# Kernel optimization log

Measured on AMD Instinct MI355X. Metric: run time of the kernel, lower is better.

Reference implementation:

```python
import jax, jax.numpy as jnp
import numpy as np

KS = 3   # deform conv kernel size
PAD = 1  # deform conv padding


def conv2d(x, w, b=None, stride=1, pad=0):
    out = jax.lax.conv_general_dilated(
        x, w, (stride, stride), [(pad, pad), (pad, pad)],
        dimension_numbers=('NCHW', 'OIHW', 'NCHW'))
    if b is not None:
        out = out + b[None, :, None, None]
    return out


def batchnorm(x, g, b, eps=1e-5):
    # training-mode BN (batch statistics, biased variance) like torch default
    m = jnp.mean(x, axis=(0, 2, 3), keepdims=True)
    v = jnp.var(x, axis=(0, 2, 3), keepdims=True)
    return (x - m) * jax.lax.rsqrt(v + eps) * g[None, :, None, None] + b[None, :, None, None]


def deform_conv(x, offset, w):
    # x: (b,c,h,w); offset: (b,2N,h,w) with first N = x-offsets, last N = y-offsets
    b, c, h, wd = x.shape
    N = KS * KS
    xp = jnp.pad(x, ((0, 0), (0, 0), (PAD, PAD), (PAD, PAD)))
    Hp, Wp = h + 2 * PAD, wd + 2 * PAD
    # kernel-point offsets p_n in {-1,0,1}^2
    r = jnp.arange(-(KS - 1) // 2, (KS - 1) // 2 + 1)
    pnx, pny = jnp.meshgrid(r, r, indexing='ij')
    p_n = jnp.concatenate([pnx.reshape(-1), pny.reshape(-1)]).astype(x.dtype)  # (2N,)
    # base sampling grid p_0 (1..h, 1..w in padded coords)
    p0x, p0y = jnp.meshgrid(jnp.arange(1, h + 1), jnp.arange(1, wd + 1), indexing='ij')
    p0 = jnp.concatenate([jnp.broadcast_to(p0x[None], (N, h, wd)),
                          jnp.broadcast_to(p0y[None], (N, h, wd))], 0).astype(x.dtype)
    p = p0[None] + p_n[None, :, None, None] + offset          # (b,2N,h,w)
    p = jnp.transpose(p, (0, 2, 3, 1))                        # (b,h,w,2N)
    px, py = p[..., :N], p[..., N:]
    fx, fy = jnp.floor(px), jnp.floor(py)
    q_ltx = jnp.clip(fx, 0, Hp - 1)
    q_lty = jnp.clip(fy, 0, Wp - 1)
    q_rbx = jnp.clip(fx + 1, 0, Hp - 1)
    q_rby = jnp.clip(fy + 1, 0, Wp - 1)
    # out-of-bound positions snapped to floor, then clamped (matches torch ref)
    mx = (px < PAD) | (px > Hp - 1 - PAD)
    my = (py < PAD) | (py > Wp - 1 - PAD)
    px = jnp.clip(jnp.where(mx, fx, px), 0, Hp - 1)
    py = jnp.clip(jnp.where(my, fy, py), 0, Wp - 1)
    g_lt = (1 + (q_ltx - px)) * (1 + (q_lty - py))
    g_rb = (1 - (q_rbx - px)) * (1 - (q_rby - py))
    g_lb = (1 + (q_ltx - px)) * (1 - (q_rby - py))
    g_rt = (1 - (q_rbx - px)) * (1 + (q_lty - py))
    x_flat = xp.reshape(b, c, Hp * Wp)

    def gather(qx, qy):
        idx = (qx.astype(jnp.int32) * Wp + qy.astype(jnp.int32)).reshape(b, 1, -1)
        out = jnp.take_along_axis(x_flat, jnp.broadcast_to(idx, (b, c, idx.shape[-1])), axis=2)
        return out.reshape(b, c, h, wd, N)

    x_off = (g_lt[:, None] * gather(q_ltx, q_lty)
             + g_rb[:, None] * gather(q_rbx, q_rby)
             + g_lb[:, None] * gather(q_ltx, q_rby)
             + g_rt[:, None] * gather(q_rbx, q_lty))   # (b,c,h,w,N)
    # (b,c,h,w,ki,kj) -> (b,c,h*ks,w*ks), then conv with stride ks
    x_off = x_off.reshape(b, c, h, wd, KS, KS).transpose(0, 1, 2, 4, 3, 5).reshape(b, c, h * KS, wd * KS)
    return conv2d(x_off, w, None, stride=KS, pad=0)


def setup_inputs() -> dict:
    key = jax.random.key(0)
    ks = jax.random.split(key, 6)
    f32 = jnp.float32
    x = jax.random.normal(ks[0], (4, 3, 224, 224), f32)
    conv1_w = jax.random.normal(ks[1], (64, 3, 3, 3), f32) * (1.0 / np.sqrt(3 * 9))
    conv1_b = jnp.zeros((64,), f32)
    bn1_g = jnp.ones((64,), f32); bn1_b = jnp.zeros((64,), f32)
    conv2_w = jax.random.normal(ks[2], (128, 64, 3, 3), f32) * (1.0 / np.sqrt(64 * 9))
    conv2_b = jnp.zeros((128,), f32)
    bn2_g = jnp.ones((128,), f32); bn2_b = jnp.zeros((128,), f32)
    off_w = jax.random.normal(ks[3], (18, 128, 3, 3), f32) * 0.01
    off_b = jnp.zeros((18,), f32)
    conv4_w = jax.random.normal(ks[4], (128, 128, 3, 3), f32) * (1.0 / np.sqrt(128 * 9))
    return {'x': x, 'conv1_w': conv1_w, 'conv1_b': conv1_b, 'bn1_g': bn1_g, 'bn1_b': bn1_b,
            'conv2_w': conv2_w, 'conv2_b': conv2_b, 'bn2_g': bn2_g, 'bn2_b': bn2_b,
            'off_w': off_w, 'off_b': off_b, 'conv4_w': conv4_w}


def reference(x, conv1_w, conv1_b, bn1_g, bn1_b, conv2_w, conv2_b, bn2_g, bn2_b, off_w, off_b, conv4_w):
    h = jax.nn.relu(conv2d(x, conv1_w, conv1_b, pad=1))
    h = batchnorm(h, bn1_g, bn1_b)
    b_, c_, H, W = h.shape
    h = h.reshape(b_, c_, H // 2, 2, W // 2, 2).mean(axis=(3, 5))  # AvgPool2d(2,2)
    h = jax.nn.relu(conv2d(h, conv2_w, conv2_b, pad=1))
    h = batchnorm(h, bn2_g, bn2_b)
    offsets = conv2d(h, off_w, off_b, pad=1)
    return deform_conv(h, offsets, conv4_w)
```

## Files before the change

### kernel.cpp

```cpp
#include <hip/hip_runtime.h>

#define HW1 50176
#define HW2 12544

typedef short bf16x8 __attribute__((ext_vector_type(8)));
typedef float f32x4  __attribute__((ext_vector_type(4)));

static __device__ __forceinline__ unsigned short f2bf(float f) {
  union { float f; unsigned int u; } v; v.f = f;
  unsigned int u = v.u;
  return (unsigned short)((u + 0x7fffu + ((u >> 16) & 1u)) >> 16);
}
static __device__ __forceinline__ float bf2f(unsigned short h) {
  union { unsigned int u; float f; } v; v.u = ((unsigned int)h) << 16;
  return v.f;
}

__global__ __launch_bounds__(256) void prep_kernel(
    const float* __restrict__ conv4_w, const float* __restrict__ conv2_w,
    const float* __restrict__ off_w,
    unsigned short* __restrict__ wbf, unsigned short* __restrict__ wb2h,
    unsigned short* __restrict__ wb2l, unsigned short* __restrict__ wboh,
    unsigned short* __restrict__ wbol)
{
  int t = blockIdx.x * 256 + threadIdx.x;
  if (t < 147456) {
    int o = t / 1152, r = t % 1152;
    int kk = r / 128, c = r % 128;
    wbf[t] = f2bf(conv4_w[((size_t)o * 128 + c) * 9 + kk]);
  }
  int t2 = t - 147456;
  if (t2 >= 0 && t2 < 73728) {
    int o = t2 / 576, r = t2 % 576;
    int kk = r / 64, c = r % 64;
    float v = conv2_w[((size_t)o * 64 + c) * 9 + kk];
    unsigned short h = f2bf(v);
    wb2h[t2] = h; wb2l[t2] = f2bf(v - bf2f(h));
  }
  int t3 = t - (147456 + 73728);
  if (t3 >= 0 && t3 < 36864) {
    int o = t3 / 1152, r = t3 % 1152;
    int kk = r / 128, c = r % 128;
    float v = (o < 18) ? off_w[((size_t)o * 128 + c) * 9 + kk] : 0.f;
    unsigned short h = f2bf(v);
    wboh[t3] = h; wbol[t3] = f2bf(v - bf2f(h));
  }
}

__global__ __launch_bounds__(256) void conv1_tiled_kernel(
    const float* __restrict__ x, const float* __restrict__ w,
    const float* __restrict__ bias, float* __restrict__ out)
{
  __shared__ float in_s[3][18][18];
  int tid = threadIdx.x;
  int tx = tid & 15, ty = tid >> 4;
  int tx0 = (blockIdx.x % 14) * 16, ty0 = (blockIdx.x / 14) * 16;
  int b = blockIdx.y;

  for (int t = tid; t < 972; t += 256) {
    int c = t / 324, r2 = t % 324;
    int r = r2 / 18, col = r2 % 18;
    int yy = ty0 + r - 1, xx = tx0 + col - 1;
    float v = 0.f;
    if (yy >= 0 && yy < 224 && xx >= 0 && xx < 224)
      v = x[((size_t)(b * 3 + c) * 224 + yy) * 224 + xx];
    in_s[c][r][col] = v;
  }
  __syncthreads();

  float xv[27];
  #pragma unroll
  for (int c = 0; c < 3; ++c)
    #pragma unroll
    for (int ky = 0; ky < 3; ++ky)
      #pragma unroll
      for (int kx = 0; kx < 3; ++kx)
        xv[c * 9 + ky * 3 + kx] = in_s[c][ty + ky][tx + kx];

  int oy = ty0 + ty, ox = tx0 + tx;
  size_t obase = ((size_t)b * 64) * HW1 + (size_t)oy * 224 + ox;
  for (int o0 = 0; o0 < 64; o0 += 16) {
    float acc[16];
    #pragma unroll
    for (int oi = 0; oi < 16; ++oi) acc[oi] = bias[o0 + oi];
    #pragma unroll
    for (int oi = 0; oi < 16; ++oi) {
      const float* wp = w + (size_t)(o0 + oi) * 27;
      #pragma unroll
      for (int k = 0; k < 27; ++k)
        acc[oi] += xv[k] * wp[k];
    }
    #pragma unroll
    for (int oi = 0; oi < 16; ++oi)
      out[obase + (size_t)(o0 + oi) * HW1] = fmaxf(acc[oi], 0.f);
  }
}

__global__ __launch_bounds__(256) void bn_stats_part_kernel(
    const float* __restrict__ in, float* __restrict__ part, int C, int HW)
{
  int c = blockIdx.y;
  int NB = gridDim.x;
  float s = 0.f, s2 = 0.f;
  int stride = NB * 256;
  int start = blockIdx.x * 256 + threadIdx.x;
  for (int b = 0; b < 4; ++b) {
    const float* p = in + (size_t)(b * C + c) * HW;
    for (int i = start; i < HW; i += stride) {
      float v = p[i];
      s += v; s2 += v * v;
    }
  }
  #pragma unroll
  for (int off = 32; off > 0; off >>= 1) {
    s  += __shfl_down(s, off, 64);
    s2 += __shfl_down(s2, off, 64);
  }
  __shared__ float red[8];
  int wid = threadIdx.x >> 6, lane = threadIdx.x & 63;
  if (lane == 0) { red[wid * 2] = s; red[wid * 2 + 1] = s2; }
  __syncthreads();
  if (threadIdx.x == 0) {
    float ts = 0.f, ts2 = 0.f;
    for (int i = 0; i < 4; ++i) { ts += red[i * 2]; ts2 += red[i * 2 + 1]; }
    part[((size_t)c * NB + blockIdx.x) * 2]     = ts;
    part[((size_t)c * NB + blockIdx.x) * 2 + 1] = ts2;
  }
}

__global__ void bn_finalize_kernel(const float* __restrict__ part, int NB,
                                   const float* __restrict__ g,
                                   const float* __restrict__ bb,
                                   float inv_n, float* __restrict__ ss, int C)
{
  int c = threadIdx.x;
  if (c < C) {
    float s = 0.f, s2 = 0.f;
    for (int i = 0; i < NB; ++i) {
      s  += part[((size_t)c * NB + i) * 2];
      s2 += part[((size_t)c * NB + i) * 2 + 1];
    }
    float m = s * inv_n;
    float v = s2 * inv_n - m * m;
    float sc = rsqrtf(v + 1e-5f) * g[c];
    ss[2 * c] = sc;
    ss[2 * c + 1] = bb[c] - m * sc;
  }
}

__global__ __launch_bounds__(256) void bn1_pool_nhwc_kernel(
    const float* __restrict__ h1, const float* __restrict__ ss,
    float* __restrict__ out)
{
  __shared__ float tile[16][65];
  int b = blockIdx.z, y = blockIdx.y, x0 = blockIdx.x * 16;
  int tid = threadIdx.x;
  int c = tid >> 2, g = tid & 3;
  const float2* r0 = (const float2*)(h1 + ((size_t)((b * 64 + c) * 224 + 2 * y)) * 224);
  const float2* r1 = r0 + 112;
  float sc = ss[2 * c], sh = ss[2 * c + 1];
  #pragma unroll
  for (int i = 0; i < 4; ++i) {
    int xl = g * 4 + i;
    float2 a = r0[x0 + xl], d = r1[x0 + xl];
    tile[xl][c] = (a.x + a.y + d.x + d.y) * 0.25f * sc + sh;
  }
  __syncthreads();
  int c2 = tid & 63, pg = tid >> 6;
  size_t obase = (size_t)b * HW2 + y * 112 + x0;
  #pragma unroll
  for (int i = 0; i < 4; ++i) {
    int xl = pg * 4 + i;
    out[(obase + xl) * 64 + c2] = tile[xl][c2];
  }
}

__global__ __launch_bounds__(256) void bn2_apply_nhwc_kernel(
    const float* __restrict__ h3, const float* __restrict__ ss,
    float* __restrict__ onhwc)
{
  __shared__ float tile[16][129];
  int b = blockIdx.z, y = blockIdx.y, x0 = blockIdx.x * 16;
  int tid = threadIdx.x;
  int xx = tid & 15, cbase = tid >> 4;
  #pragma unroll
  for (int it = 0; it < 8; ++it) {
    int c = cbase + it * 16;
    size_t gi = ((size_t)((b * 128 + c) * 112 + y)) * 112 + x0 + xx;
    tile[xx][c] = h3[gi] * ss[2 * c] + ss[2 * c + 1];
  }
  __syncthreads();
  int c2 = tid & 127, xb2 = tid >> 7;
  #pragma unroll
  for (int it = 0; it < 8; ++it) {
    int xx2 = xb2 + it * 2;
    onhwc[((size_t)((b * 112 + y) * 112) + x0 + xx2) * 128 + c2] = tile[xx2][c2];
  }
}

__global__ __launch_bounds__(256) void conv2_mfma3_kernel(
    const float* __restrict__ xin, const unsigned short* __restrict__ wh,
    const unsigned short* __restrict__ wl, const float* __restrict__ bias,
    float* __restrict__ out)
{
  __shared__ unsigned short wh_lds[128 * 32];
  __shared__ unsigned short wl_lds[128 * 32];
  __shared__ unsigned short xh_lds[64 * 32];
  __shared__ unsigned short xl_lds[64 * 32];
  int tid = threadIdx.x;
  int hw = blockIdx.y * 196 + blockIdx.x;
  int swz = (hw & 7) * 98 + (hw >> 3);
  int p0 = (swz % 196) * 64;
  int b  = swz / 196;
  const float* xb = xin + (size_t)b * HW2 * 64;

  f32x4 acc[4][2];
  #pragma unroll
  for (int f = 0; f < 4; ++f)
    #pragma unroll
    for (int g = 0; g < 2; ++g)
      acc[f][g] = (f32x4){0.f, 0.f, 0.f, 0.f};

  int wid = tid >> 6, l = tid & 63;
  int wo = (wid & 1) * 64, wp = (wid >> 1) * 32;
  int kgl = l >> 4, rl = l & 15;

  int pl = tid >> 2, kg = tid & 3;
  int pix = p0 + pl;
  int pi = pix / 112, pj = pix % 112;

  for (int step = 0; step < 18; ++step) {
    int k0 = step * 32;
    int kk = k0 >> 6;
    __syncthreads();
    #pragma unroll
    for (int it = 0; it < 2; ++it) {
      int task = tid + it * 256;
      int row = task >> 2, wkg = task & 3;
      size_t goff = (size_t)row * 576 + k0 + wkg * 8;
      int loff = row * 32 + ((wkg ^ ((row >> 1) & 3)) << 3);
      *(bf16x8*)(wh_lds + loff) = *(const bf16x8*)(wh + goff);
      *(bf16x8*)(wl_lds + loff) = *(const bf16x8*)(wl + goff);
    }
    {
      int dy = kk / 3 - 1, dx = kk % 3 - 1;
      int yy = pi + dy, xx = pj + dx;
      int c = (k0 & 63) + kg * 8;
      bf16x8 xvh, xvl;
      if (yy >= 0 && yy < 112 && xx >= 0 && xx < 112) {
        const float4* tp = (const float4*)(xb + ((size_t)(yy * 112 + xx)) * 64 + c);
        float4 t0 = tp[0], t1 = tp[1];
        float v[8] = {t0.x, t0.y, t0.z, t0.w, t1.x, t1.y, t1.z, t1.w};
        #pragma unroll
        for (int t = 0; t < 8; ++t) {
          unsigned short hsh = f2bf(v[t]);
          xvh[t] = (short)hsh;
          xvl[t] = (short)f2bf(v[t] - bf2f(hsh));
        }
      } else {
        #pragma unroll
        for (int t = 0; t < 8; ++t) { xvh[t] = 0; xvl[t] = 0; }
      }
      int loff = pl * 32 + ((kg ^ ((pl >> 1) & 3)) << 3);
      *(bf16x8*)(xh_lds + loff) = xvh;
      *(bf16x8*)(xl_lds + loff) = xvl;
    }
    __syncthreads();
    bf16x8 ah[4], al[4], bh[2], bl[2];
    #pragma unroll
    for (int f = 0; f < 4; ++f) {
      int r = wo + f * 16 + rl;
      int loff = r * 32 + ((kgl ^ ((r >> 1) & 3)) << 3);
      ah[f] = *(const bf16x8*)(wh_lds + loff);
      al[f] = *(const bf16x8*)(wl_lds + loff);
    }
    #pragma unroll
    for (int g = 0; g < 2; ++g) {
      int r = wp + g * 16 + rl;
      int loff = r * 32 + ((kgl ^ ((r >> 1) & 3)) << 3);
      bh[g] = *(const bf16x8*)(xh_lds + loff);
      bl[g] = *(const bf16x8*)(xl_lds + loff);
    }
    #pragma unroll
    for (int f = 0; f < 4; ++f)
      #pragma unroll
      for (int g = 0; g < 2; ++g) {
        acc[f][g] = __builtin_amdgcn_mfma_f32_16x16x32_bf16(ah[f], bh[g], acc[f][g], 0, 0, 0);
        acc[f][g] = __builtin_amdgcn_mfma_f32_16x16x32_bf16(ah[f], bl[g], acc[f][g], 0, 0, 0);
        acc[f][g] = __builtin_amdgcn_mfma_f32_16x16x32_bf16(al[f], bh[g], acc[f][g], 0, 0, 0);
      }
  }

  int jrow = (l >> 4) * 4, col = l & 15;
  #pragma unroll
  for (int f = 0; f < 4; ++f) {
    #pragma unroll
    for (int g = 0; g < 2; ++g) {
      int p = p0 + wp + g * 16 + col;
      #pragma unroll
      for (int j = 0; j < 4; ++j) {
        int o = wo + f * 16 + jrow + j;
        out[((size_t)(b * 128 + o)) * HW2 + p] = fmaxf(acc[f][g][j] + bias[o], 0.f);
      }
    }
  }
}

__global__ __launch_bounds__(256) void off_mfma3_kernel(
    const float* __restrict__ xin, const unsigned short* __restrict__ wh,
    const unsigned short* __restrict__ wl, const float* __restrict__ bias,
    float* __restrict__ out)
{
  __shared__ unsigned short wh_lds[32 * 32];
  __shared__ unsigned short wl_lds[32 * 32];
  __shared__ unsigned short xh_lds[128 * 32];
  __shared__ unsigned short xl_lds[128 * 32];
  int tid = threadIdx.x;
  int hw = blockIdx.y * 98 + blockIdx.x;
  int swz = (hw & 7) * 49 + (hw >> 3);
  int p0 = (swz % 98) * 128;
  int b  = swz / 98;
  const float* xb = xin + (size_t)b * HW2 * 128;

  f32x4 acc[2][2];
  #pragma unroll
  for (int f = 0; f < 2; ++f)
    #pragma unroll
    for (int g = 0; g < 2; ++g)
      acc[f][g] = (f32x4){0.f, 0.f, 0.f, 0.f};

  int wid = tid >> 6, l = tid & 63;
  int wp = wid * 32;
  int kgl = l >> 4, rl = l & 15;

  for (int step = 0; step < 36; ++step) {
    int k0 = step * 32;
    int kk = k0 >> 7;
    int dy = kk / 3 - 1, dx = kk % 3 - 1;
    __syncthreads();
    if (tid < 128) {
      int row = tid >> 2, wkg = tid & 3;
      size_t goff = (size_t)row * 1152 + k0 + wkg * 8;
      int loff = row * 32 + ((wkg ^ ((row >> 1) & 3)) << 3);
      *(bf16x8*)(wh_lds + loff) = *(const bf16x8*)(wh + goff);
      *(bf16x8*)(wl_lds + loff) = *(const bf16x8*)(wl + goff);
    }
    #pragma unroll
    for (int it = 0; it < 2; ++it) {
      int task = tid + it * 256;
      int pl = task >> 2, kg = task & 3;
      int pix = p0 + pl;
      int pi = pix / 112, pj = pix % 112;
      int yy = pi + dy, xx = pj + dx;
      int c = (k0 & 127) + kg * 8;
      bf16x8 xvh, xvl;
      if (yy >= 0 && yy < 112 && xx >= 0 && xx < 112) {
        const float4* tp = (const float4*)(xb + ((size_t)(yy * 112 + xx)) * 128 + c);
        float4 t0 = tp[0], t1 = tp[1];
        float v[8] = {t0.x, t0.y, t0.z, t0.w, t1.x, t1.y, t1.z, t1.w};
        #pragma unroll
        for (int t = 0; t < 8; ++t) {
          unsigned short hsh = f2bf(v[t]);
          xvh[t] = (short)hsh;
          xvl[t] = (short)f2bf(v[t] - bf2f(hsh));
        }
      } else {
        #pragma unroll
        for (int t = 0; t < 8; ++t) { xvh[t] = 0; xvl[t] = 0; }
      }
      int loff = pl * 32 + ((kg ^ ((pl >> 1) & 3)) << 3);
      *(bf16x8*)(xh_lds + loff) = xvh;
      *(bf16x8*)(xl_lds + loff) = xvl;
    }
    __syncthreads();
    bf16x8 ah[2], al[2], bh[2], bl[2];
    #pragma unroll
    for (int f = 0; f < 2; ++f) {
      int r = f * 16 + rl;
      int loff = r * 32 + ((kgl ^ ((r >> 1) & 3)) << 3);
      ah[f] = *(const bf16x8*)(wh_lds + loff);
      al[f] = *(const bf16x8*)(wl_lds + loff);
    }
    #pragma unroll
    for (int g = 0; g < 2; ++g) {
      int r = wp + g * 16 + rl;
      int loff = r * 32 + ((kgl ^ ((r >> 1) & 3)) << 3);
      bh[g] = *(const bf16x8*)(xh_lds + loff);
      bl[g] = *(const bf16x8*)(xl_lds + loff);
    }
    #pragma unroll
    for (int f = 0; f < 2; ++f)
      #pragma unroll
      for (int g = 0; g < 2; ++g) {
        acc[f][g] = __builtin_amdgcn_mfma_f32_16x16x32_bf16(ah[f], bh[g], acc[f][g], 0, 0, 0);
        acc[f][g] = __builtin_amdgcn_mfma_f32_16x16x32_bf16(ah[f], bl[g], acc[f][g], 0, 0, 0);
        acc[f][g] = __builtin_amdgcn_mfma_f32_16x16x32_bf16(al[f], bh[g], acc[f][g], 0, 0, 0);
      }
  }

  int jrow = (l >> 4) * 4, col = l & 15;
  #pragma unroll
  for (int f = 0; f < 2; ++f) {
    #pragma unroll
    for (int g = 0; g < 2; ++g) {
      int p = p0 + wp + g * 16 + col;
      #pragma unroll
      for (int j = 0; j < 4; ++j) {
        int o = f * 16 + jrow + j;
        if (o < 18)
          out[((size_t)(b * 18 + o)) * HW2 + p] = acc[f][g][j] + bias[o];
      }
    }
  }
}

__global__ __launch_bounds__(256) void deform_mfma_kernel(
    const float* __restrict__ xin, const float* __restrict__ offs,
    const unsigned short* __restrict__ wb, float* __restrict__ out)
{
  __shared__ int            idx_s[576][4];
  __shared__ float          wt_s[576][4];
  __shared__ unsigned short w_lds[128 * 64];
  __shared__ unsigned short x_lds[64 * 64];

  int tid = threadIdx.x;
  int hw = blockIdx.y * 196 + blockIdx.x;
  int swz = (hw & 7) * 98 + (hw >> 3);
  int p0 = (swz % 196) * 64;
  int b  = swz / 196;
  const float* xb = xin + (size_t)b * HW2 * 128;

  for (int t = tid; t < 576; t += 256) {
    int p = t / 9, k = t % 9;
    int pix = p0 + p;
    int i = pix / 112, j = pix % 112;
    float offx = offs[((size_t)(b * 18 + k) * 112 + i) * 112 + j];
    float offy = offs[((size_t)(b * 18 + 9 + k) * 112 + i) * 112 + j];
    float px = (float)(i + k / 3) + offx;
    float py = (float)(j + k % 3) + offy;
    float fx = floorf(px), fy = floorf(py);
    float qltx = fminf(fmaxf(fx, 0.f), 113.f);
    float qlty = fminf(fmaxf(fy, 0.f), 113.f);
    float qrbx = fminf(fmaxf(fx + 1.f, 0.f), 113.f);
    float qrby = fminf(fmaxf(fy + 1.f, 0.f), 113.f);
    bool mx = (px < 1.f) || (px > 112.f);
    bool my = (py < 1.f) || (py > 112.f);
    float pxc = fminf(fmaxf(mx ? fx : px, 0.f), 113.f);
    float pyc = fminf(fmaxf(my ? fy : py, 0.f), 113.f);
    float glt = (1.f + (qltx - pxc)) * (1.f + (qlty - pyc));
    float grb = (1.f - (qrbx - pxc)) * (1.f - (qrby - pyc));
    float glb = (1.f + (qltx - pxc)) * (1.f - (qrby - pyc));
    float grt = (1.f - (qrbx - pxc)) * (1.f + (qlty - pyc));
    int ix0 = (int)qltx - 1, iy0 = (int)qlty - 1;
    int ix1 = (int)qrbx - 1, iy1 = (int)qrby - 1;
    bool vx0 = (ix0 >= 0 && ix0 < 112), vy0 = (iy0 >= 0 && iy0 < 112);
    bool vx1 = (ix1 >= 0 && ix1 < 112), vy1 = (iy1 >= 0 && iy1 < 112);
    idx_s[t][0] = (vx0 && vy0) ? ix0 * 112 + iy0 : -1;  wt_s[t][0] = glt;
    idx_s[t][1] = (vx1 && vy1) ? ix1 * 112 + iy1 : -1;  wt_s[t][1] = grb;
    idx_s[t][2] = (vx0 && vy1) ? ix0 * 112 + iy1 : -1;  wt_s[t][2] = glb;
    idx_s[t][3] = (vx1 && vy0) ? ix1 * 112 + iy0 : -1;  wt_s[t][3] = grt;
  }

  f32x4 acc[4][2];
  #pragma unroll
  for (int f = 0; f < 4; ++f)
    #pragma unroll
    for (int g = 0; g < 2; ++g)
      acc[f][g] = (f32x4){0.f, 0.f, 0.f, 0.f};

  int wid = tid >> 6;
  int l   = tid & 63;
  int wo = (wid & 1) * 64;
  int wp = (wid >> 1) * 32;
  int kgl = l >> 4;
  int rl  = l & 15;

  for (int step = 0; step < 18; ++step) {
    int k0 = step * 64;
    int kk = step >> 1;
    int c0 = (step & 1) * 64;
    __syncthreads();

    #pragma unroll
    for (int it = 0; it < 4; ++it) {
      int task = tid + it * 256;
      int row = task >> 3, kg8 = task & 7;
      int sub = kg8 >> 2, kg = kg8 & 3;
      bf16x8 wv = *(const bf16x8*)(wb + (size_t)row * 1152 + k0 + sub * 32 + kg * 8);
      *(bf16x8*)(w_lds + row * 64 + sub * 32 + ((kg ^ ((row >> 1) & 3)) << 3)) = wv;
    }

    {
      int pl = tid >> 2, kg = tid & 3;
      int c = c0 + kg * 8;
      int pk = pl * 9 + kk;
      float v0 = 0.f, v1 = 0.f, v2 = 0.f, v3 = 0.f;
      float v4 = 0.f, v5 = 0.f, v6 = 0.f, v7 = 0.f;
      float u0 = 0.f, u1 = 0.f, u2 = 0.f, u3 = 0.f;
      float u4 = 0.f, u5 = 0.f, u6 = 0.f, u7 = 0.f;
      #pragma unroll
      for (int q = 0; q < 4; ++q) {
        int s = idx_s[pk][q];
        if (s >= 0) {
          float wq = wt_s[pk][q];
          const float4* tp = (const float4*)(xb + (size_t)s * 128 + c);
          float4 t0 = tp[0], t1 = tp[1], t2 = tp[8], t3 = tp[9];
          v0 += wq * t0.x; v1 += wq * t0.y; v2 += wq * t0.z; v3 += wq * t0.w;
          v4 += wq * t1.x; v5 += wq * t1.y; v6 += wq * t1.z; v7 += wq * t1.w;
          u0 += wq * t2.x; u1 += wq * t2.y; u2 += wq * t2.z; u3 += wq * t2.w;
          u4 += wq * t3.x; u5 += wq * t3.y; u6 += wq * t3.z; u7 += wq * t3.w;
        }
      }
      bf16x8 xv, xu;
      xv[0] = (short)f2bf(v0); xv[1] = (short)f2bf(v1);
      xv[2] = (short)f2bf(v2); xv[3] = (short)f2bf(v3);
      xv[4] = (short)f2bf(v4); xv[5] = (short)f2bf(v5);
      xv[6] = (short)f2bf(v6); xv[7] = (short)f2bf(v7);
      xu[0] = (short)f2bf(u0); xu[1] = (short)f2bf(u1);
      xu[2] = (short)f2bf(u2); xu[3] = (short)f2bf(u3);
      xu[4] = (short)f2bf(u4); xu[5] = (short)f2bf(u5);
      xu[6] = (short)f2bf(u6); xu[7] = (short)f2bf(u7);
      int sw = ((kg ^ ((pl >> 1) & 3)) << 3);
      *(bf16x8*)(x_lds + pl * 64 + sw) = xv;
      *(bf16x8*)(x_lds + pl * 64 + 32 + sw) = xu;
    }
    __syncthreads();

    #pragma unroll
    for (int sub = 0; sub < 2; ++sub) {
      bf16x8 af[4], bx[2];
      #pragma unroll
      for (int f = 0; f < 4; ++f) {
        int r = wo + f * 16 + rl;
        af[f] = *(const bf16x8*)(w_lds + r * 64 + sub * 32 + ((kgl ^ ((r >> 1) & 3)) << 3));
      }
      #pragma unroll
      for (int g = 0; g < 2; ++g) {
        int r = wp + g * 16 + rl;
        bx[g] = *(const bf16x8*)(x_lds + r * 64 + sub * 32 + ((kgl ^ ((r >> 1) & 3)) << 3));
      }
      #pragma unroll
      for (int f = 0; f < 4; ++f)
        #pragma unroll
        for (int g = 0; g < 2; ++g)
          acc[f][g] = __builtin_amdgcn_mfma_f32_16x16x32_bf16(af[f], bx[g], acc[f][g], 0, 0, 0);
    }
  }

  int jrow = (l >> 4) * 4;
  int col  = l & 15;
  #pragma unroll
  for (int f = 0; f < 4; ++f) {
    #pragma unroll
    for (int g = 0; g < 2; ++g) {
      #pragma unroll
      for (int j = 0; j < 4; ++j) {
        int o = wo + f * 16 + jrow + j;
        int p = p0 + wp + g * 16 + col;
        out[((size_t)(b * 128 + o)) * HW2 + p] = acc[f][g][j];
      }
    }
  }
}

extern "C" void kernel_launch(void* const* d_in, const int* in_sizes, int n_in,
                              void* d_out, int out_size, void* d_ws, size_t ws_size,
                              hipStream_t stream)
{
  const float* x       = (const float*)d_in[0];
  const float* conv1_w = (const float*)d_in[1];
  const float* conv1_b = (const float*)d_in[2];
  const float* bn1_g   = (const float*)d_in[3];
  const float* bn1_b   = (const float*)d_in[4];
  const float* conv2_w = (const float*)d_in[5];
  const float* conv2_b = (const float*)d_in[6];
  const float* bn2_g   = (const float*)d_in[7];
  const float* bn2_b   = (const float*)d_in[8];
  const float* off_w   = (const float*)d_in[9];
  const float* off_b   = (const float*)d_in[10];
  const float* conv4_w = (const float*)d_in[11];
  float* out = (float*)d_out;
  float* ws  = (float*)d_ws;

  float* bufA  = ws;
  float* bufB  = bufA + 12845056;
  float* bufC  = bufB + 3211264;
  float* offsb = bufC + 6422528;
  float* part  = offsb + 903168;
  float* ss    = part + 8192;
  unsigned short* wbf  = (unsigned short*)(ss + 384);
  unsigned short* wb2h = wbf + 147456;
  unsigned short* wb2l = wb2h + 73728;
  unsigned short* wboh = wb2l + 73728;
  unsigned short* wbol = wboh + 36864;

  float* h1  = bufA;
  float* h2t = bufB;
  float* h3  = bufA;
  float* h4t = bufC;
  float* part1 = part;
  float* part2 = part + 4096;

  prep_kernel<<<1008, 256, 0, stream>>>(conv4_w, conv2_w, off_w,
                                        wbf, wb2h, wb2l, wboh, wbol);

  conv1_tiled_kernel<<<dim3(196, 4), 256, 0, stream>>>(x, conv1_w, conv1_b, h1);
  bn_stats_part_kernel<<<dim3(32, 64), 256, 0, stream>>>(h1, part1, 64, HW1);
  bn_finalize_kernel<<<1, 128, 0, stream>>>(part1, 32, bn1_g, bn1_b, 1.f / (4.f * HW1), ss, 64);
  bn1_pool_nhwc_kernel<<<dim3(7, 112, 4), 256, 0, stream>>>(h1, ss, h2t);

  conv2_mfma3_kernel<<<dim3(196, 4), 256, 0, stream>>>(h2t, wb2h, wb2l, conv2_b, h3);
  bn_stats_part_kernel<<<dim3(16, 128), 256, 0, stream>>>(h3, part2, 128, HW2);
  bn_finalize_kernel<<<1, 128, 0, stream>>>(part2, 16, bn2_g, bn2_b, 1.f / (4.f * HW2), ss + 128, 128);
  bn2_apply_nhwc_kernel<<<dim3(7, 112, 4), 256, 0, stream>>>(h3, ss + 128, h4t);

  off_mfma3_kernel<<<dim3(98, 4), 256, 0, stream>>>(h4t, wboh, wbol, off_b, offsb);
  deform_mfma_kernel<<<dim3(196, 4), 256, 0, stream>>>(h4t, offsb, wbf, out);
}
```

Measured before the change: 319.3 us.

## Fuse BN2 statistics into conv2 epilogue, emit NHWC and bf16 copy for deform gather

Conv2 now writes its output directly in NHWC layout and computes per-channel sum and sum-of-squares partials with wave shuffles and LDS, which removes the separate stats pass. The transpose kernel is replaced by an elementwise BN apply that writes both fp32 NHWC (for the offset conv) and a bf16 NHWC copy. The deform kernel gathers the bf16 copy, halving gather bytes, and stores indices as shorts in LDS. The trade-offs are a finalize over 784 partials per channel, an extra bf16 output write, and reduced precision of the sampled inputs.

```diff
diff --git a/kernel.cpp b/kernel.cpp
--- a/kernel.cpp
+++ b/kernel.cpp
@@ -4,6 +4,7 @@
 #define HW2 12544
 
 typedef short bf16x8 __attribute__((ext_vector_type(8)));
+typedef short bf16x4 __attribute__((ext_vector_type(4)));
 typedef float f32x4  __attribute__((ext_vector_type(4)));
 
 static __device__ __forceinline__ unsigned short f2bf(float f) {
@@ -175,38 +176,16 @@
   }
 }
 
-__global__ __launch_bounds__(256) void bn2_apply_nhwc_kernel(
-    const float* __restrict__ h3, const float* __restrict__ ss,
-    float* __restrict__ onhwc)
-{
-  __shared__ float tile[16][129];
-  int b = blockIdx.z, y = blockIdx.y, x0 = blockIdx.x * 16;
-  int tid = threadIdx.x;
-  int xx = tid & 15, cbase = tid >> 4;
-  #pragma unroll
-  for (int it = 0; it < 8; ++it) {
-    int c = cbase + it * 16;
-    size_t gi = ((size_t)((b * 128 + c) * 112 + y)) * 112 + x0 + xx;
-    tile[xx][c] = h3[gi] * ss[2 * c] + ss[2 * c + 1];
-  }
-  __syncthreads();
-  int c2 = tid & 127, xb2 = tid >> 7;
-  #pragma unroll
-  for (int it = 0; it < 8; ++it) {
-    int xx2 = xb2 + it * 2;
-    onhwc[((size_t)((b * 112 + y) * 112) + x0 + xx2) * 128 + c2] = tile[xx2][c2];
-  }
-}
-
 __global__ __launch_bounds__(256) void conv2_mfma3_kernel(
     const float* __restrict__ xin, const unsigned short* __restrict__ wh,
     const unsigned short* __restrict__ wl, const float* __restrict__ bias,
-    float* __restrict__ out)
+    float* __restrict__ out, float* __restrict__ part)
 {
   __shared__ unsigned short wh_lds[128 * 32];
   __shared__ unsigned short wl_lds[128 * 32];
   __shared__ unsigned short xh_lds[64 * 32];
   __shared__ unsigned short xl_lds[64 * 32];
+  __shared__ float bred[2][2][128];
   int tid = threadIdx.x;
   int hw = blockIdx.y * 196 + blockIdx.x;
   int swz = (hw & 7) * 98 + (hw >> 3);
@@ -292,18 +271,75 @@
   }
 
   int jrow = (l >> 4) * 4, col = l & 15;
+  float sv[4][4], sq[4][4];
+  #pragma unroll
+  for (int f = 0; f < 4; ++f)
+    #pragma unroll
+    for (int j = 0; j < 4; ++j) { sv[f][j] = 0.f; sq[f][j] = 0.f; }
+
   #pragma unroll
   for (int f = 0; f < 4; ++f) {
+    int ob = wo + f * 16 + jrow;
     #pragma unroll
     for (int g = 0; g < 2; ++g) {
       int p = p0 + wp + g * 16 + col;
+      float4 vv;
+      float* pv = &vv.x;
+      #pragma unroll
+      for (int j = 0; j < 4; ++j) {
+        float val = fmaxf(acc[f][g][j] + bias[ob + j], 0.f);
+        pv[j] = val;
+        sv[f][j] += val;
+        sq[f][j] += val * val;
+      }
+      *(float4*)(out + ((size_t)b * HW2 + p) * 128 + ob) = vv;
+    }
+  }
+  #pragma unroll
+  for (int off = 1; off < 16; off <<= 1) {
+    #pragma unroll
+    for (int f = 0; f < 4; ++f)
+      #pragma unroll
+      for (int j = 0; j < 4; ++j) {
+        sv[f][j] += __shfl_xor(sv[f][j], off, 64);
+        sq[f][j] += __shfl_xor(sq[f][j], off, 64);
+      }
+  }
+  if ((l & 15) == 0) {
+    int ph = wid >> 1;
+    #pragma unroll
+    for (int f = 0; f < 4; ++f)
       #pragma unroll
       for (int j = 0; j < 4; ++j) {
         int o = wo + f * 16 + jrow + j;
-        out[((size_t)(b * 128 + o)) * HW2 + p] = fmaxf(acc[f][g][j] + bias[o], 0.f);
-      }
-    }
-  }
+        bred[ph][0][o] = sv[f][j];
+        bred[ph][1][o] = sq[f][j];
+      }
+  }
+  __syncthreads();
+  if (tid < 128) {
+    part[((size_t)tid * 784 + swz) * 2]     = bred[0][0][tid] + bred[1][0][tid];
+    part[((size_t)tid * 784 + swz) * 2 + 1] = bred[0][1][tid] + bred[1][1][tid];
+  }
+}
+
+__global__ __launch_bounds__(256) void bn2_elem_kernel(
+    const float* __restrict__ in, const float* __restrict__ ss,
+    float* __restrict__ of32, unsigned short* __restrict__ obf)
+{
+  int idx = blockIdx.x * 256 + threadIdx.x;
+  if (idx >= 4 * HW2 * 32) return;
+  int c0 = (idx & 31) * 4;
+  float4 v = ((const float4*)in)[idx];
+  v.x = v.x * ss[2 * c0]     + ss[2 * c0 + 1];
+  v.y = v.y * ss[2 * c0 + 2] + ss[2 * c0 + 3];
+  v.z = v.z * ss[2 * c0 + 4] + ss[2 * c0 + 5];
+  v.w = v.w * ss[2 * c0 + 6] + ss[2 * c0 + 7];
+  ((float4*)of32)[idx] = v;
+  bf16x4 bv;
+  bv[0] = (short)f2bf(v.x); bv[1] = (short)f2bf(v.y);
+  bv[2] = (short)f2bf(v.z); bv[3] = (short)f2bf(v.w);
+  *(bf16x4*)(obf + (size_t)idx * 4) = bv;
 }
 
 __global__ __launch_bounds__(256) void off_mfma3_kernel(
@@ -415,10 +451,10 @@
 }
 
 __global__ __launch_bounds__(256) void deform_mfma_kernel(
-    const float* __restrict__ xin, const float* __restrict__ offs,
+    const unsigned short* __restrict__ xin, const float* __restrict__ offs,
     const unsigned short* __restrict__ wb, float* __restrict__ out)
 {
-  __shared__ int            idx_s[576][4];
+  __shared__ short          idx_s[576][4];
   __shared__ float          wt_s[576][4];
   __shared__ unsigned short w_lds[128 * 64];
   __shared__ unsigned short x_lds[64 * 64];
@@ -428,7 +464,7 @@
   int swz = (hw & 7) * 98 + (hw >> 3);
   int p0 = (swz % 196) * 64;
   int b  = swz / 196;
-  const float* xb = xin + (size_t)b * HW2 * 128;
+  const unsigned short* xb = xin + (size_t)b * HW2 * 128;
 
   for (int t = tid; t < 576; t += 256) {
     int p = t / 9, k = t % 9;
@@ -455,10 +491,10 @@
     int ix1 = (int)qrbx - 1, iy1 = (int)qrby - 1;
     bool vx0 = (ix0 >= 0 && ix0 < 112), vy0 = (iy0 >= 0 && iy0 < 112);
     bool vx1 = (ix1 >= 0 && ix1 < 112), vy1 = (iy1 >= 0 && iy1 < 112);
-    idx_s[t][0] = (vx0 && vy0) ? ix0 * 112 + iy0 : -1;  wt_s[t][0] = glt;
-    idx_s[t][1] = (vx1 && vy1) ? ix1 * 112 + iy1 : -1;  wt_s[t][1] = grb;
-    idx_s[t][2] = (vx0 && vy1) ? ix0 * 112 + iy1 : -1;  wt_s[t][2] = glb;
-    idx_s[t][3] = (vx1 && vy0) ? ix1 * 112 + iy0 : -1;  wt_s[t][3] = grt;
+    idx_s[t][0] = (short)((vx0 && vy0) ? ix0 * 112 + iy0 : -1);  wt_s[t][0] = glt;
+    idx_s[t][1] = (short)((vx1 && vy1) ? ix1 * 112 + iy1 : -1);  wt_s[t][1] = grb;
+    idx_s[t][2] = (short)((vx0 && vy1) ? ix0 * 112 + iy1 : -1);  wt_s[t][2] = glb;
+    idx_s[t][3] = (short)((vx1 && vy0) ? ix1 * 112 + iy0 : -1);  wt_s[t][3] = grt;
   }
 
   f32x4 acc[4][2];
@@ -503,12 +539,16 @@
         int s = idx_s[pk][q];
         if (s >= 0) {
           float wq = wt_s[pk][q];
-          const float4* tp = (const float4*)(xb + (size_t)s * 128 + c);
-          float4 t0 = tp[0], t1 = tp[1], t2 = tp[8], t3 = tp[9];
-          v0 += wq * t0.x; v1 += wq * t0.y; v2 += wq * t0.z; v3 += wq * t0.w;
-          v4 += wq * t1.x; v5 += wq * t1.y; v6 += wq * t1.z; v7 += wq * t1.w;
-          u0 += wq * t2.x; u1 += wq * t2.y; u2 += wq * t2.z; u3 += wq * t2.w;
-          u4 += wq * t3.x; u5 += wq * t3.y; u6 += wq * t3.z; u7 += wq * t3.w;
+          const bf16x8* tp = (const bf16x8*)(xb + (size_t)s * 128 + c);
+          bf16x8 t0 = tp[0], t1 = tp[4];
+          v0 += wq * bf2f((unsigned short)t0[0]); v1 += wq * bf2f((unsigned short)t0[1]);
+          v2 += wq * bf2f((unsigned short)t0[2]); v3 += wq * bf2f((unsigned short)t0[3]);
+          v4 += wq * bf2f((unsigned short)t0[4]); v5 += wq * bf2f((unsigned short)t0[5]);
+          v6 += wq * bf2f((unsigned short)t0[6]); v7 += wq * bf2f((unsigned short)t0[7]);
+          u0 += wq * bf2f((unsigned short)t1[0]); u1 += wq * bf2f((unsigned short)t1[1]);
+          u2 += wq * bf2f((unsigned short)t1[2]); u3 += wq * bf2f((unsigned short)t1[3]);
+          u4 += wq * bf2f((unsigned short)t1[4]); u5 += wq * bf2f((unsigned short)t1[5]);
+          u6 += wq * bf2f((unsigned short)t1[6]); u7 += wq * bf2f((unsigned short)t1[7]);
         }
       }
       bf16x8 xv, xu;
@@ -586,8 +626,9 @@
   float* bufB  = bufA + 12845056;
   float* bufC  = bufB + 3211264;
   float* offsb = bufC + 6422528;
-  float* part  = offsb + 903168;
-  float* ss    = part + 8192;
+  float* part1 = offsb + 903168;
+  float* part2 = part1 + 4096;
+  float* ss    = part2 + 200704;
   unsigned short* wbf  = (unsigned short*)(ss + 384);
   unsigned short* wb2h = wbf + 147456;
   unsigned short* wb2l = wb2h + 73728;
@@ -596,10 +637,9 @@
 
   float* h1  = bufA;
   float* h2t = bufB;
-  float* h3  = bufA;
+  float* h3t = bufA;
   float* h4t = bufC;
-  float* part1 = part;
-  float* part2 = part + 4096;
+  unsigned short* h4b = (unsigned short*)bufB;
 
   prep_kernel<<<1008, 256, 0, stream>>>(conv4_w, conv2_w, off_w,
                                         wbf, wb2h, wb2l, wboh, wbol);
@@ -609,11 +649,10 @@
   bn_finalize_kernel<<<1, 128, 0, stream>>>(part1, 32, bn1_g, bn1_b, 1.f / (4.f * HW1), ss, 64);
   bn1_pool_nhwc_kernel<<<dim3(7, 112, 4), 256, 0, stream>>>(h1, ss, h2t);
 
-  conv2_mfma3_kernel<<<dim3(196, 4), 256, 0, stream>>>(h2t, wb2h, wb2l, conv2_b, h3);
-  bn_stats_part_kernel<<<dim3(16, 128), 256, 0, stream>>>(h3, part2, 128, HW2);
-  bn_finalize_kernel<<<1, 128, 0, stream>>>(part2, 16, bn2_g, bn2_b, 1.f / (4.f * HW2), ss + 128, 128);
-  bn2_apply_nhwc_kernel<<<dim3(7, 112, 4), 256, 0, stream>>>(h3, ss + 128, h4t);
+  conv2_mfma3_kernel<<<dim3(196, 4), 256, 0, stream>>>(h2t, wb2h, wb2l, conv2_b, h3t, part2);
+  bn_finalize_kernel<<<1, 128, 0, stream>>>(part2, 784, bn2_g, bn2_b, 1.f / (4.f * HW2), ss + 128, 128);
+  bn2_elem_kernel<<<(4 * HW2 * 32 + 255) / 256, 256, 0, stream>>>(h3t, ss + 128, h4t, h4b);
 
   off_mfma3_kernel<<<dim3(98, 4), 256, 0, stream>>>(h4t, wboh, wbol, off_b, offsb);
-  deform_mfma_kernel<<<dim3(196, 4), 256, 0, stream>>>(h4t, offsb, wbf, out);
-}
+  deform_mfma_kernel<<<dim3(196, 4), 256, 0, stream>>>(h4b, offsb, wbf, out);
+}
```

Result: slower. 372.6 us (+16.7%).
